# Optimization experiments

Measured on AMD Instinct MI355X. Metric: run time of the kernel, lower is better.

Reference implementation:

```python
import jax, jax.numpy as jnp
import numpy as np

WIDTH, HEIGHT = 96, 72
DIST_COEF = 0.1  # CARLA

# CARLA intrinsics per options_from_source: fx=fy=cx=width/2, cy=height/2
_K = np.array([[48.0, 48.0, 0.0], [36.0, 0.0, 36.0], [1.0, 0.0, 0.0]], dtype=np.float64)
_invK = np.linalg.inv(_K)
_u = np.arange(WIDTH, dtype=np.float64)
_v = np.arange(HEIGHT, dtype=np.float64)
_uu = np.tile(_u, (HEIGHT, 1)).reshape(-1)
_vv = np.repeat(_v, WIDTH)
_uv1 = np.stack([_uu, _vv, np.ones_like(_uu)], axis=0)  # (3, N)
YZ1_GRID = jnp.asarray((_invK @ _uv1).astype(np.float32))  # (3, N)


def setup_inputs() -> dict:
    key = jax.random.key(0)
    k1, k2, k3, k4, k5, k6 = jax.random.split(key, 6)
    B = 1
    # depths strictly positive so the depth>0 mask keeps every pixel (dense, jit-friendly)
    depth1 = jax.random.uniform(k1, (B, 1, HEIGHT, WIDTH), jnp.float32) * 5.0 + 0.1
    depth2 = jax.random.uniform(k2, (B, 1, HEIGHT, WIDTH), jnp.float32) * 5.0 + 0.1
    img1 = jax.random.normal(k3, (B, 3, HEIGHT, WIDTH), jnp.float32)
    img2 = jax.random.normal(k4, (B, 3, HEIGHT, WIDTH), jnp.float32)
    # near-identity rigid-ish transforms (valid homogeneous poses)
    eye = jnp.eye(4, dtype=jnp.float32)[None]
    noise1 = 0.01 * jax.random.normal(k5, (B, 4, 4), jnp.float32)
    noise2 = 0.01 * jax.random.normal(k6, (B, 4, 4), jnp.float32)
    bottom = jnp.zeros((B, 1, 4), jnp.float32).at[:, 0, 3].set(1.0)
    pose1_2 = jnp.concatenate([(eye + noise1)[:, :3, :], bottom], axis=1)
    pose1_2_gt = jnp.concatenate([(eye + noise2)[:, :3, :], bottom], axis=1)
    return {"depth1": depth1, "depth2": depth2, "pose1_2": pose1_2,
            "img1": img1, "img2": img2, "pose1_2_gt": pose1_2_gt}


def _kern_sum(a, b, gram):
    # a: (B,3,N), b: (B,3,M), gram: (B,N,M)
    # sum over n,m of exp(-||a_n - b_m||^2 * dist_coef) * gram[n,m]
    sq = (jnp.sum(a * a, axis=1)[:, :, None]
          + jnp.sum(b * b, axis=1)[:, None, :]
          - 2.0 * jnp.einsum('bcn,bcm->bnm', a, b))
    return jnp.sum(jnp.exp(-sq * DIST_COEF) * gram, axis=(1, 2))  # (B,)


def _transform(pose, xyz):
    # pose: (B,4,4), xyz: (B,3,N) -> rotated+translated points (B,3,N)
    return jnp.einsum('bij,bjn->bin', pose[:, :3, :3], xyz) + pose[:, :3, 3:4]


def reference(depth1, depth2, pose1_2, img1, img2, pose1_2_gt):
    B = depth1.shape[0]
    d1 = depth1.reshape(B, 1, -1)  # (B,1,N)
    d2 = depth2.reshape(B, 1, -1)
    f1 = img1.reshape(B, 3, -1)    # (B,3,N)
    f2 = img2.reshape(B, 3, -1)

    xyz1 = YZ1_GRID[None] * d1     # (B,3,N) back-projected points
    xyz2 = YZ1_GRID[None] * d2
    xyz2_t = _transform(pose1_2, xyz2)
    xyz2_tgt = _transform(pose1_2_gt, xyz2)

    # gramian(..., norm_mode=False, kernalize=False) -> plain feature inner products
    g11 = jnp.einsum('bcn,bcm->bnm', f1, f1)
    g22 = jnp.einsum('bcn,bcm->bnm', f2, f2)
    g12 = jnp.einsum('bcn,bcm->bnm', f1, f2)

    f1_f1 = _kern_sum(xyz1, xyz1, g11)
    f2_f2 = _kern_sum(xyz2_t, xyz2_t, g22)
    f1_f2 = _kern_sum(xyz1, xyz2_t, g12)
    f2_f2_gt = _kern_sum(xyz2_tgt, xyz2_tgt, g22)
    f1_f2_gt = _kern_sum(xyz1, xyz2_tgt, g12)

    inner_neg = f1_f1 + f2_f2 - 2.0 * f1_f2
    inner_neg_gt = f1_f1 + f2_f2_gt - 2.0 * f1_f2_gt
    return jnp.sum(inner_neg / inner_neg_gt)  # scalar, summed over batch
```

## Files before the change

kernel.cpp:

```cpp
#include <hip/hip_runtime.h>

typedef float v2f __attribute__((ext_vector_type(2)));

constexpr int WIDTH  = 96;
constexpr int HEIGHT = 72;
constexpr int NPTS   = WIDTH * HEIGHT;

constexpr int BLOCK  = 128;
constexpr int NTILE  = 256;
constexpr int MTILE  = 64;
constexpr int NTB    = NPTS / NTILE;
constexpr int MTB    = NPTS / MTILE;
constexpr int NBF    = NTB * MTB;

constexpr int TT     = 128;
constexpr int T      = NPTS / TT;
constexpr int NBT    = T * (T + 1) / 2;

constexpr int NBLK   = NBT + NBF;

constexpr int ROWT   = 20;
constexpr int ROWFN  = 8;
constexpr int ROWFM  = 12;

constexpr float KEXP  = -0.14426950408889634f;
constexpr float M2K   = -2.0f * KEXP;

__global__ __launch_bounds__(256) void precompute_kernel(
    const float* __restrict__ depth1, const float* __restrict__ depth2,
    const float* __restrict__ pose,   const float* __restrict__ img1,
    const float* __restrict__ img2,   const float* __restrict__ poseg,
    float* __restrict__ QT, float* __restrict__ QFn, float* __restrict__ QFm)
{
    const int idx = blockIdx.x * 256 + threadIdx.x;

    float R[12], G[12];
#pragma unroll
    for (int i = 0; i < 12; ++i) { R[i] = pose[i]; G[i] = poseg[i]; }

    const int u = idx % WIDTH;
    const int v = idx / WIDTH;
    const float gy = (float)u * (1.0f / 48.0f) - 1.0f;
    const float gz = (float)v * (1.0f / 36.0f) - 1.0f;
    const float d1 = depth1[idx];
    const float d2 = depth2[idx];
    const float x1 = d1, y1 = d1 * gy, z1 = d1 * gz;
    const float x2 = d2, y2 = d2 * gy, z2 = d2 * gz;
    const float xt = R[0] * x2 + R[1] * y2 + R[2]  * z2 + R[3];
    const float yt = R[4] * x2 + R[5] * y2 + R[6]  * z2 + R[7];
    const float zt = R[8] * x2 + R[9] * y2 + R[10] * z2 + R[11];
    const float xg = G[0] * x2 + G[1] * y2 + G[2]  * z2 + G[3];
    const float yg = G[4] * x2 + G[5] * y2 + G[6]  * z2 + G[7];
    const float zg = G[8] * x2 + G[9] * y2 + G[10] * z2 + G[11];

    const float q1 = KEXP * (x1*x1 + y1*y1 + z1*z1);
    const float qt = KEXP * (xt*xt + yt*yt + zt*zt);
    const float qg = KEXP * (xg*xg + yg*yg + zg*zg);
    const float f1a = img1[idx], f1b = img1[NPTS + idx], f1c = img1[2*NPTS + idx];
    const float f2a = img2[idx], f2b = img2[NPTS + idx], f2c = img2[2*NPTS + idx];

    float4* qt_row = (float4*)(QT + (size_t)idx * ROWT);
    qt_row[0] = make_float4(x1, y1, z1, q1);
    qt_row[1] = make_float4(xt, yt, zt, qt);
    qt_row[2] = make_float4(xg, yg, zg, qg);
    qt_row[3] = make_float4(f1a, f1b, f1c, f2a);
    qt_row[4] = make_float4(f2b, f2c, 0.f, 0.f);

    float4* fn_row = (float4*)(QFn + (size_t)idx * ROWFN);
    fn_row[0] = make_float4(M2K * x1, M2K * y1, M2K * z1, q1);
    fn_row[1] = make_float4(f1a, f1b, f1c, 0.f);

    float4* fm_row = (float4*)(QFm + (size_t)idx * ROWFM);
    fm_row[0] = make_float4(xt, yt, zt, qt);
    fm_row[1] = make_float4(xg, yg, zg, qg);
    fm_row[2] = make_float4(f2a, f2b, f2c, 0.f);
}

__global__ __launch_bounds__(BLOCK) void pair_kernel(
    const float* __restrict__ QT,  const float* __restrict__ QFn,
    const float* __restrict__ QFm,
    float* __restrict__ pT, float* __restrict__ pF)
{
    __shared__ float red[2][3];
    const int t = threadIdx.x;

    if (blockIdx.x < NBT) {
        int rem = blockIdx.x, i = 0;
        while (rem >= T - i) { rem -= T - i; ++i; }
        const int j = i + rem;

        float A[18];
        {
            const float4* r = (const float4*)(QT + (size_t)(i * TT + t) * ROWT);
            const float4 w0 = r[0], w1 = r[1], w2 = r[2], w3 = r[3], w4 = r[4];
            A[0]=M2K*w0.x; A[1]=M2K*w0.y; A[2]=M2K*w0.z; A[3]=w0.w;
            A[4]=M2K*w1.x; A[5]=M2K*w1.y; A[6]=M2K*w1.z; A[7]=w1.w;
            A[8]=M2K*w2.x; A[9]=M2K*w2.y; A[10]=M2K*w2.z; A[11]=w2.w;
            A[12]=w3.x; A[13]=w3.y; A[14]=w3.z;
            A[15]=w3.w; A[16]=w4.x; A[17]=w4.y;
        }

        float s0 = 0.f, s1 = 0.f, s3 = 0.f;
        const float* __restrict__ q0 = QT + (size_t)(j * TT) * ROWT;
#pragma unroll 2
        for (int m = 0; m < TT; ++m) {
            const float* __restrict__ b = q0 + m * ROWT;
            float t11 = A[3] + b[3];
            t11 = A[0] * b[0] + t11;
            t11 = A[1] * b[1] + t11;
            t11 = A[2] * b[2] + t11;
            float t22 = A[7] + b[7];
            t22 = A[4] * b[4] + t22;
            t22 = A[5] * b[5] + t22;
            t22 = A[6] * b[6] + t22;
            float tgg = A[11] + b[11];
            tgg = A[8]  * b[8]  + tgg;
            tgg = A[9]  * b[9]  + tgg;
            tgg = A[10] * b[10] + tgg;
            float g11 = A[12] * b[12];
            g11 = A[13] * b[13] + g11;
            g11 = A[14] * b[14] + g11;
            float g22 = A[15] * b[15];
            g22 = A[16] * b[16] + g22;
            g22 = A[17] * b[17] + g22;
            const float e11 = __builtin_amdgcn_exp2f(t11);
            const float e22 = __builtin_amdgcn_exp2f(t22);
            const float egg = __builtin_amdgcn_exp2f(tgg);
            s0 = e11 * g11 + s0;
            s1 = e22 * g22 + s1;
            s3 = egg * g22 + s3;
        }
        const float w = (i == j) ? 1.f : 2.f;
        s0 *= w; s1 *= w; s3 *= w;

#pragma unroll
        for (int off = 32; off > 0; off >>= 1) {
            s0 += __shfl_down(s0, off);
            s1 += __shfl_down(s1, off);
            s3 += __shfl_down(s3, off);
        }
        const int wave = t >> 6, lane = t & 63;
        if (lane == 0) { red[wave][0]=s0; red[wave][1]=s1; red[wave][2]=s3; }
        __syncthreads();
        if (t == 0) {
            pT[0 * NBT + blockIdx.x] = red[0][0] + red[1][0];
            pT[1 * NBT + blockIdx.x] = red[0][1] + red[1][1];
            pT[2 * NBT + blockIdx.x] = red[0][2] + red[1][2];
        }
    } else {
        const int blk = blockIdx.x - NBT;
        const int bn = blk % NTB;
        const int bm = blk / NTB;

        v2f A[7];
        {
            const int n0 = bn * NTILE + t;
            const float4* r0 = (const float4*)(QFn + (size_t)n0 * ROWFN);
            const float4* r1 = (const float4*)(QFn + (size_t)(n0 + BLOCK) * ROWFN);
            const float4 a0 = r0[0], a1 = r0[1], c0 = r1[0], c1 = r1[1];
            A[0].x=a0.x; A[0].y=c0.x;  A[1].x=a0.y; A[1].y=c0.y;
            A[2].x=a0.z; A[2].y=c0.z;  A[3].x=a0.w; A[3].y=c0.w;
            A[4].x=a1.x; A[4].y=c1.x;  A[5].x=a1.y; A[5].y=c1.y;
            A[6].x=a1.z; A[6].y=c1.z;
        }

        v2f s2 = {0.f, 0.f}, s4 = s2;
        const float* __restrict__ q0 = QFm + (size_t)(bm * MTILE) * ROWFM;
#pragma unroll 2
        for (int m = 0; m < MTILE; ++m) {
            const float* __restrict__ b = q0 + m * ROWFM;
            v2f t12 = A[3] + b[3];
            t12 = A[0] * b[0] + t12;
            t12 = A[1] * b[1] + t12;
            t12 = A[2] * b[2] + t12;
            v2f t1g = A[3] + b[7];
            t1g = A[0] * b[4] + t1g;
            t1g = A[1] * b[5] + t1g;
            t1g = A[2] * b[6] + t1g;
            v2f g12 = A[4] * b[8];
            g12 = A[5] * b[9]  + g12;
            g12 = A[6] * b[10] + g12;
            v2f e12, e1g;
            e12.x = __builtin_amdgcn_exp2f(t12.x);
            e12.y = __builtin_amdgcn_exp2f(t12.y);
            e1g.x = __builtin_amdgcn_exp2f(t1g.x);
            e1g.y = __builtin_amdgcn_exp2f(t1g.y);
            s2 = e12 * g12 + s2;
            s4 = e1g * g12 + s4;
        }

        float r2 = s2.x + s2.y, r4 = s4.x + s4.y;
#pragma unroll
        for (int off = 32; off > 0; off >>= 1) {
            r2 += __shfl_down(r2, off);
            r4 += __shfl_down(r4, off);
        }
        const int wave = t >> 6, lane = t & 63;
        if (lane == 0) { red[wave][0] = r2; red[wave][1] = r4; }
        __syncthreads();
        if (t == 0) {
            pF[0 * NBF + blk] = red[0][0] + red[1][0];
            pF[1 * NBF + blk] = red[0][1] + red[1][1];
        }
    }
}

__global__ __launch_bounds__(256) void finalize_kernel(
    const float* __restrict__ pT, const float* __restrict__ pF,
    float* __restrict__ out)
{
    __shared__ double red[4][5];
    double l0 = 0, l1 = 0, l2 = 0, l3 = 0, l4 = 0;
    for (int b = threadIdx.x; b < NBT; b += 256) {
        l0 += pT[0 * NBT + b];
        l1 += pT[1 * NBT + b];
        l3 += pT[2 * NBT + b];
    }
    for (int b = threadIdx.x; b < NBF; b += 256) {
        l2 += pF[0 * NBF + b];
        l4 += pF[1 * NBF + b];
    }
#pragma unroll
    for (int off = 32; off > 0; off >>= 1) {
        l0 += __shfl_down(l0, off);
        l1 += __shfl_down(l1, off);
        l2 += __shfl_down(l2, off);
        l3 += __shfl_down(l3, off);
        l4 += __shfl_down(l4, off);
    }
    const int wave = threadIdx.x >> 6, lane = threadIdx.x & 63;
    if (lane == 0) {
        red[wave][0] = l0; red[wave][1] = l1; red[wave][2] = l2;
        red[wave][3] = l3; red[wave][4] = l4;
    }
    __syncthreads();
    if (threadIdx.x == 0) {
        const double a0 = red[0][0] + red[1][0] + red[2][0] + red[3][0];
        const double a1 = red[0][1] + red[1][1] + red[2][1] + red[3][1];
        const double a2 = red[0][2] + red[1][2] + red[2][2] + red[3][2];
        const double a3 = red[0][3] + red[1][3] + red[2][3] + red[3][3];
        const double a4 = red[0][4] + red[1][4] + red[2][4] + red[3][4];
        const double num = a0 + a1 - 2.0 * a2;
        const double den = a0 + a3 - 2.0 * a4;
        out[0] = (float)(num / den);
    }
}

extern "C" void kernel_launch(void* const* d_in, const int* in_sizes, int n_in,
                              void* d_out, int out_size, void* d_ws, size_t ws_size,
                              hipStream_t stream)
{
    const float* depth1 = (const float*)d_in[0];
    const float* depth2 = (const float*)d_in[1];
    const float* pose   = (const float*)d_in[2];
    const float* img1   = (const float*)d_in[3];
    const float* img2   = (const float*)d_in[4];
    const float* poseg  = (const float*)d_in[5];

    float* QT  = (float*)d_ws;
    float* QFn = QT  + (size_t)NPTS * ROWT;
    float* QFm = QFn + (size_t)NPTS * ROWFN;
    float* pT  = QFm + (size_t)NPTS * ROWFM;
    float* pF  = pT  + 3 * NBT;

    precompute_kernel<<<NPTS / 256, 256, 0, stream>>>(depth1, depth2, pose,
                                                      img1, img2, poseg,
                                                      QT, QFn, QFm);
    pair_kernel<<<NBLK, BLOCK, 0, stream>>>(QT, QFn, QFm, pT, pF);
    finalize_kernel<<<1, 256, 0, stream>>>(pT, pF, (float*)d_out);
}
```

Before: 58.16 us.

## Process two/three rows per thread in pair kernel to amortize column loads

The triangular self-pair path now handles two rows per thread with packed v2f math (TT raised to 256), and the cross-pair path handles three rows per thread (NTILE raised to 384, a packed pair plus one scalar row). Each loaded column row is reused across more accumulations, which cuts memory loads per FLOP and block count, and lets packed FMA instructions be used. In exchange register pressure rises and there are fewer blocks, which may hurt occupancy and load balance on a small problem.

```diff
diff --git a/kernel.cpp b/kernel.cpp
--- a/kernel.cpp
+++ b/kernel.cpp
@@ -7,15 +7,16 @@
 constexpr int NPTS   = WIDTH * HEIGHT;
 
 constexpr int BLOCK  = 128;
-constexpr int NTILE  = 256;
+
+constexpr int TT     = 256;
+constexpr int T      = NPTS / TT;
+constexpr int NBT    = T * (T + 1) / 2;
+
+constexpr int NTILE  = 384;
 constexpr int MTILE  = 64;
 constexpr int NTB    = NPTS / NTILE;
 constexpr int MTB    = NPTS / MTILE;
 constexpr int NBF    = NTB * MTB;
-
-constexpr int TT     = 128;
-constexpr int T      = NPTS / TT;
-constexpr int NBT    = T * (T + 1) / 2;
 
 constexpr int NBLK   = NBT + NBF;
 
@@ -89,58 +90,72 @@
         while (rem >= T - i) { rem -= T - i; ++i; }
         const int j = i + rem;
 
-        float A[18];
+        v2f A[18];
         {
-            const float4* r = (const float4*)(QT + (size_t)(i * TT + t) * ROWT);
-            const float4 w0 = r[0], w1 = r[1], w2 = r[2], w3 = r[3], w4 = r[4];
-            A[0]=M2K*w0.x; A[1]=M2K*w0.y; A[2]=M2K*w0.z; A[3]=w0.w;
-            A[4]=M2K*w1.x; A[5]=M2K*w1.y; A[6]=M2K*w1.z; A[7]=w1.w;
-            A[8]=M2K*w2.x; A[9]=M2K*w2.y; A[10]=M2K*w2.z; A[11]=w2.w;
-            A[12]=w3.x; A[13]=w3.y; A[14]=w3.z;
-            A[15]=w3.w; A[16]=w4.x; A[17]=w4.y;
-        }
-
-        float s0 = 0.f, s1 = 0.f, s3 = 0.f;
+            const float4* r0 = (const float4*)(QT + (size_t)(i * TT + t) * ROWT);
+            const float4* r1 = (const float4*)(QT + (size_t)(i * TT + BLOCK + t) * ROWT);
+#pragma unroll
+            for (int g = 0; g < 3; ++g) {
+                const float4 w0 = r0[g], w1 = r1[g];
+                A[4*g+0].x = M2K*w0.x; A[4*g+0].y = M2K*w1.x;
+                A[4*g+1].x = M2K*w0.y; A[4*g+1].y = M2K*w1.y;
+                A[4*g+2].x = M2K*w0.z; A[4*g+2].y = M2K*w1.z;
+                A[4*g+3].x = w0.w;     A[4*g+3].y = w1.w;
+            }
+            const float4 w30 = r0[3], w31 = r1[3];
+            const float4 w40 = r0[4], w41 = r1[4];
+            A[12].x=w30.x; A[12].y=w31.x;  A[13].x=w30.y; A[13].y=w31.y;
+            A[14].x=w30.z; A[14].y=w31.z;  A[15].x=w30.w; A[15].y=w31.w;
+            A[16].x=w40.x; A[16].y=w41.x;  A[17].x=w40.y; A[17].y=w41.y;
+        }
+
+        v2f s0 = {0.f, 0.f}, s1 = s0, s3 = s0;
         const float* __restrict__ q0 = QT + (size_t)(j * TT) * ROWT;
 #pragma unroll 2
         for (int m = 0; m < TT; ++m) {
             const float* __restrict__ b = q0 + m * ROWT;
-            float t11 = A[3] + b[3];
+            v2f t11 = A[3] + b[3];
             t11 = A[0] * b[0] + t11;
             t11 = A[1] * b[1] + t11;
             t11 = A[2] * b[2] + t11;
-            float t22 = A[7] + b[7];
+            v2f t22 = A[7] + b[7];
             t22 = A[4] * b[4] + t22;
             t22 = A[5] * b[5] + t22;
             t22 = A[6] * b[6] + t22;
-            float tgg = A[11] + b[11];
+            v2f tgg = A[11] + b[11];
             tgg = A[8]  * b[8]  + tgg;
             tgg = A[9]  * b[9]  + tgg;
             tgg = A[10] * b[10] + tgg;
-            float g11 = A[12] * b[12];
+            v2f g11 = A[12] * b[12];
             g11 = A[13] * b[13] + g11;
             g11 = A[14] * b[14] + g11;
-            float g22 = A[15] * b[15];
+            v2f g22 = A[15] * b[15];
             g22 = A[16] * b[16] + g22;
             g22 = A[17] * b[17] + g22;
-            const float e11 = __builtin_amdgcn_exp2f(t11);
-            const float e22 = __builtin_amdgcn_exp2f(t22);
-            const float egg = __builtin_amdgcn_exp2f(tgg);
+            v2f e11, e22, egg;
+            e11.x = __builtin_amdgcn_exp2f(t11.x);
+            e11.y = __builtin_amdgcn_exp2f(t11.y);
+            e22.x = __builtin_amdgcn_exp2f(t22.x);
+            e22.y = __builtin_amdgcn_exp2f(t22.y);
+            egg.x = __builtin_amdgcn_exp2f(tgg.x);
+            egg.y = __builtin_amdgcn_exp2f(tgg.y);
             s0 = e11 * g11 + s0;
             s1 = e22 * g22 + s1;
             s3 = egg * g22 + s3;
         }
         const float w = (i == j) ? 1.f : 2.f;
-        s0 *= w; s1 *= w; s3 *= w;
+        float r0 = w * (s0.x + s0.y);
+        float r1 = w * (s1.x + s1.y);
+        float r3 = w * (s3.x + s3.y);
 
 #pragma unroll
         for (int off = 32; off > 0; off >>= 1) {
-            s0 += __shfl_down(s0, off);
-            s1 += __shfl_down(s1, off);
-            s3 += __shfl_down(s3, off);
+            r0 += __shfl_down(r0, off);
+            r1 += __shfl_down(r1, off);
+            r3 += __shfl_down(r3, off);
         }
         const int wave = t >> 6, lane = t & 63;
-        if (lane == 0) { red[wave][0]=s0; red[wave][1]=s1; red[wave][2]=s3; }
+        if (lane == 0) { red[wave][0]=r0; red[wave][1]=r1; red[wave][2]=r3; }
         __syncthreads();
         if (t == 0) {
             pT[0 * NBT + blockIdx.x] = red[0][0] + red[1][0];
@@ -152,44 +167,68 @@
         const int bn = blk % NTB;
         const int bm = blk / NTB;
 
-        v2f A[7];
+        v2f A2[7];  float A1[7];
         {
             const int n0 = bn * NTILE + t;
             const float4* r0 = (const float4*)(QFn + (size_t)n0 * ROWFN);
             const float4* r1 = (const float4*)(QFn + (size_t)(n0 + BLOCK) * ROWFN);
-            const float4 a0 = r0[0], a1 = r0[1], c0 = r1[0], c1 = r1[1];
-            A[0].x=a0.x; A[0].y=c0.x;  A[1].x=a0.y; A[1].y=c0.y;
-            A[2].x=a0.z; A[2].y=c0.z;  A[3].x=a0.w; A[3].y=c0.w;
-            A[4].x=a1.x; A[4].y=c1.x;  A[5].x=a1.y; A[5].y=c1.y;
-            A[6].x=a1.z; A[6].y=c1.z;
-        }
-
-        v2f s2 = {0.f, 0.f}, s4 = s2;
+            const float4* r2 = (const float4*)(QFn + (size_t)(n0 + 2*BLOCK) * ROWFN);
+            const float4 a0 = r0[0], a1 = r0[1];
+            const float4 c0 = r1[0], c1 = r1[1];
+            const float4 d0 = r2[0], d1 = r2[1];
+            A2[0].x=a0.x; A2[0].y=c0.x;  A2[1].x=a0.y; A2[1].y=c0.y;
+            A2[2].x=a0.z; A2[2].y=c0.z;  A2[3].x=a0.w; A2[3].y=c0.w;
+            A2[4].x=a1.x; A2[4].y=c1.x;  A2[5].x=a1.y; A2[5].y=c1.y;
+            A2[6].x=a1.z; A2[6].y=c1.z;
+            A1[0]=d0.x; A1[1]=d0.y; A1[2]=d0.z; A1[3]=d0.w;
+            A1[4]=d1.x; A1[5]=d1.y; A1[6]=d1.z;
+        }
+
+        v2f s2v = {0.f, 0.f}, s4v = s2v;
+        float s2s = 0.f, s4s = 0.f;
         const float* __restrict__ q0 = QFm + (size_t)(bm * MTILE) * ROWFM;
 #pragma unroll 2
         for (int m = 0; m < MTILE; ++m) {
             const float* __restrict__ b = q0 + m * ROWFM;
-            v2f t12 = A[3] + b[3];
-            t12 = A[0] * b[0] + t12;
-            t12 = A[1] * b[1] + t12;
-            t12 = A[2] * b[2] + t12;
-            v2f t1g = A[3] + b[7];
-            t1g = A[0] * b[4] + t1g;
-            t1g = A[1] * b[5] + t1g;
-            t1g = A[2] * b[6] + t1g;
-            v2f g12 = A[4] * b[8];
-            g12 = A[5] * b[9]  + g12;
-            g12 = A[6] * b[10] + g12;
+            v2f t12 = A2[3] + b[3];
+            t12 = A2[0] * b[0] + t12;
+            t12 = A2[1] * b[1] + t12;
+            t12 = A2[2] * b[2] + t12;
+            v2f t1g = A2[3] + b[7];
+            t1g = A2[0] * b[4] + t1g;
+            t1g = A2[1] * b[5] + t1g;
+            t1g = A2[2] * b[6] + t1g;
+            v2f g12 = A2[4] * b[8];
+            g12 = A2[5] * b[9]  + g12;
+            g12 = A2[6] * b[10] + g12;
+            float u12 = A1[3] + b[3];
+            u12 = A1[0] * b[0] + u12;
+            u12 = A1[1] * b[1] + u12;
+            u12 = A1[2] * b[2] + u12;
+            float u1g = A1[3] + b[7];
+            u1g = A1[0] * b[4] + u1g;
+            u1g = A1[1] * b[5] + u1g;
+            u1g = A1[2] * b[6] + u1g;
+            float h12 = A1[4] * b[8];
+            h12 = A1[5] * b[9]  + h12;
+            h12 = A1[6] * b[10] + h12;
+
             v2f e12, e1g;
             e12.x = __builtin_amdgcn_exp2f(t12.x);
             e12.y = __builtin_amdgcn_exp2f(t12.y);
             e1g.x = __builtin_amdgcn_exp2f(t1g.x);
             e1g.y = __builtin_amdgcn_exp2f(t1g.y);
-            s2 = e12 * g12 + s2;
-            s4 = e1g * g12 + s4;
-        }
-
-        float r2 = s2.x + s2.y, r4 = s4.x + s4.y;
+            const float f12 = __builtin_amdgcn_exp2f(u12);
+            const float f1g = __builtin_amdgcn_exp2f(u1g);
+
+            s2v = e12 * g12 + s2v;
+            s4v = e1g * g12 + s4v;
+            s2s = f12 * h12 + s2s;
+            s4s = f1g * h12 + s4s;
+        }
+
+        float r2 = s2v.x + s2v.y + s2s;
+        float r4 = s4v.x + s4v.y + s4s;
 #pragma unroll
         for (int off = 32; off > 0; off >>= 1) {
             r2 += __shfl_down(r2, off);
```

Result: slower. 67.47 us (+16.0%).
